# Kernel tuning notes

Measured on AMD Instinct MI355X. Metric: run time of the kernel, lower is better.

## Reference

```python
import jax, jax.numpy as jnp
import numpy as np

B, T, I, L, D, O = 256, 512, 512, 128, 4, 2
LN_EPS = 1e-5

def setup_inputs() -> dict:
    key = jax.random.key(0)
    ks = jax.random.split(key, 7)
    x = jax.random.normal(ks[0], (B, T, I), jnp.float32)
    # Xavier-ish scaling keeps the recurrence numerically tame
    W_in = jax.random.normal(ks[1], (L, D, I), jnp.float32) * (1.0 / np.sqrt(I))
    W_liquid = jax.random.normal(ks[2], (L, D, L), jnp.float32) * (1.0 / np.sqrt(L))
    W_gate = jax.random.normal(ks[3], (L, D), jnp.float32)
    b_liquid = jnp.zeros((L,), jnp.float32)
    W_out = jax.random.normal(ks[4], (O, L), jnp.float32) * (1.0 / np.sqrt(L))
    b_out = jnp.zeros((O,), jnp.float32)
    ln_w = jnp.ones((L,), jnp.float32)
    ln_b = jnp.zeros((L,), jnp.float32)
    leaky_rate = jnp.asarray(0.3, jnp.float32)
    return {"x": x, "W_in": W_in, "W_liquid": W_liquid, "W_gate": W_gate,
            "b_liquid": b_liquid, "W_out": W_out, "b_out": b_out,
            "ln_w": ln_w, "ln_b": ln_b, "leaky_rate": leaky_rate}

def reference(x, W_in, W_liquid, W_gate, b_liquid, W_out, b_out, ln_w, ln_b, leaky_rate):
    # Liquid dendritic RNN. Dropout is identity (eval mode).
    gate = jax.nn.sigmoid(W_gate)                                   # [L,D]
    # Input branch has no recurrent dependency -> batch it over all timesteps
    in_br = jax.nn.relu(jnp.einsum('ldi,bti->btld', W_in, x))       # [B,T,L,D]
    merged_in = jnp.einsum('btld,ld->btl', in_br, gate)             # [B,T,L]
    alpha = jax.nn.sigmoid(leaky_rate)

    def step(state, m_in_t):                                        # state [B,L]
        rec_br = jax.nn.relu(jnp.einsum('ldh,bh->bld', W_liquid, state))
        merged_rec = jnp.einsum('bld,ld->bl', rec_br, gate)
        li = m_in_t + merged_rec + b_liquid                         # [B,L]
        mu = jnp.mean(li, axis=-1, keepdims=True)
        var = jnp.var(li, axis=-1, keepdims=True)
        li = (li - mu) * jax.lax.rsqrt(var + LN_EPS) * ln_w + ln_b
        new_state = (1.0 - alpha) * state + alpha * jnp.tanh(li)
        return new_state, None

    state0 = jnp.zeros((x.shape[0], W_in.shape[0]), x.dtype)
    final_state, _ = jax.lax.scan(step, state0, jnp.swapaxes(merged_in, 0, 1))
    return final_state @ W_out.T + b_out                            # [B,O]
```

## Files before the change

kernel.cpp:

```cpp
#include <hip/hip_runtime.h>
#include <hip/hip_bf16.h>
#include <stdint.h>


typedef __bf16 bf16x8 __attribute__((ext_vector_type(8)));
typedef float f32x4_t __attribute__((ext_vector_type(4)));

__device__ inline unsigned short f2bf(float f) {
    union { float f; unsigned u; } v; v.f = f;
    unsigned r = v.u + 0x7fffu + ((v.u >> 16) & 1u);
    return (unsigned short)(r >> 16);
}

__device__ inline void lds_barrier() {
    asm volatile("s_waitcnt lgkmcnt(0)" ::: "memory");
    __builtin_amdgcn_s_barrier();
}

__global__ __launch_bounds__(256, 2)
void gemm_in_kernel(const float* __restrict__ x, const float* __restrict__ W_in,
                    const float* __restrict__ W_gate, const float* __restrict__ b_liq,
                    float* __restrict__ mt)
{
    __shared__ unsigned short As[128 * 32];
    __shared__ unsigned short Bs[128 * 32];

    const int tid = threadIdx.x;
    const int m0 = blockIdx.y * 128;
    const int n0 = blockIdx.x * 128;
    const int lane = tid & 63;
    const int wid  = tid >> 6;
    const int wr = wid >> 1, wc = wid & 1;
    const int fr = lane & 15, fq = lane >> 4;

    f32x4_t acc[4][4];
    #pragma unroll
    for (int i = 0; i < 4; ++i)
        #pragma unroll
        for (int j = 0; j < 4; ++j)
            acc[i][j] = (f32x4_t){0.f, 0.f, 0.f, 0.f};

    for (int k0 = 0; k0 < 512; k0 += 32) {
        #pragma unroll
        for (int p = 0; p < 4; ++p) {
            int ch = tid + p * 256;
            int r  = ch >> 3;
            int c  = ch & 7;
            float4 va = *(const float4*)(x    + (size_t)(m0 + r) * 512 + k0 + c * 4);
            float4 vb = *(const float4*)(W_in + (size_t)(n0 + r) * 512 + k0 + c * 4);
            ushort4 ha, hb;
            ha.x = f2bf(va.x); ha.y = f2bf(va.y); ha.z = f2bf(va.z); ha.w = f2bf(va.w);
            hb.x = f2bf(vb.x); hb.y = f2bf(vb.y); hb.z = f2bf(vb.z); hb.w = f2bf(vb.w);
            *(ushort4*)(&As[r * 32 + c * 4]) = ha;
            *(ushort4*)(&Bs[r * 32 + c * 4]) = hb;
        }
        __syncthreads();

        bf16x8 af[4], bfr[4];
        #pragma unroll
        for (int mi = 0; mi < 4; ++mi)
            af[mi] = *(const bf16x8*)(&As[(wr * 64 + mi * 16 + fr) * 32 + fq * 8]);
        #pragma unroll
        for (int ni = 0; ni < 4; ++ni)
            bfr[ni] = *(const bf16x8*)(&Bs[(wc * 64 + ni * 16 + fr) * 32 + fq * 8]);

        #pragma unroll
        for (int mi = 0; mi < 4; ++mi)
            #pragma unroll
            for (int ni = 0; ni < 4; ++ni)
                acc[mi][ni] = __builtin_amdgcn_mfma_f32_16x16x32_bf16(
                                  af[mi], bfr[ni], acc[mi][ni], 0, 0, 0);
        __syncthreads();
    }

    float gv[4], blq[4];
    #pragma unroll
    for (int ni = 0; ni < 4; ++ni) {
        int n = n0 + wc * 64 + ni * 16 + fr;
        gv[ni]  = 1.f / (1.f + __expf(-W_gate[n]));
        blq[ni] = b_liq[n >> 2];
    }
    #pragma unroll
    for (int mi = 0; mi < 4; ++mi) {
        #pragma unroll
        for (int ni = 0; ni < 4; ++ni) {
            int n = n0 + wc * 64 + ni * 16 + fr;
            int l = n >> 2;
            #pragma unroll
            for (int j = 0; j < 4; ++j) {
                float v = acc[mi][ni][j];
                float r = fmaxf(v, 0.f) * gv[ni];
                r += __shfl_xor(r, 1);
                r += __shfl_xor(r, 2);
                if ((lane & 3) == 0) {
                    int row = m0 + wr * 64 + mi * 16 + fq * 4 + j;
                    int bb = row >> 9;
                    int tt = row & 511;
                    mt[(size_t)bb * 65536 + (size_t)l * 512 + tt] = r + blq[ni];
                }
            }
        }
    }
}

__global__ __launch_bounds__(256, 1)
void scan_kernel(const float* __restrict__ mt, const float* __restrict__ W_liq,
                 const float* __restrict__ W_gate, const float* __restrict__ W_out,
                 const float* __restrict__ b_out, const float* __restrict__ ln_w,
                 const float* __restrict__ ln_b, const float* __restrict__ leaky,
                 float* __restrict__ out)
{
    __shared__ __align__(16) unsigned short s_bf[128];
    __shared__ __align__(16) float red2[8];
    __shared__ float s_final[128];

    const int tid  = threadIdx.x;
    const int b    = blockIdx.x;
    const int lane = tid & 63;
    const int w    = tid >> 6;
    const int fr   = lane & 15;
    const int fq   = lane >> 4;

    bf16x8 wfrag[8][4];
    #pragma unroll
    for (int mi = 0; mi < 8; ++mi) {
        const int n = w * 128 + mi * 16 + fr;
        const float gn = 1.f / (1.f + __expf(-W_gate[n]));
        const float* wrow = W_liq + (size_t)n * 128;
        #pragma unroll
        for (int kk = 0; kk < 4; ++kk) {
            float4 f0 = *(const float4*)(wrow + kk * 32 + fq * 8);
            float4 f1 = *(const float4*)(wrow + kk * 32 + fq * 8 + 4);
            union { unsigned short u[8]; bf16x8 v; } cv;
            cv.u[0] = f2bf(gn * f0.x); cv.u[1] = f2bf(gn * f0.y);
            cv.u[2] = f2bf(gn * f0.z); cv.u[3] = f2bf(gn * f0.w);
            cv.u[4] = f2bf(gn * f1.x); cv.u[5] = f2bf(gn * f1.y);
            cv.u[6] = f2bf(gn * f1.z); cv.u[7] = f2bf(gn * f1.w);
            wfrag[mi][kk] = cv.v;
        }
    }

    size_t midx[8];
    #pragma unroll
    for (int mi = 0; mi < 8; ++mi)
        midx[mi] = (size_t)b * 65536 + (size_t)(w * 32 + mi * 4 + fq) * 512;

    const int l_own  = w * 32 + (fr & 7) * 4 + fq;
    const float lw_o = ln_w[l_own];
    const float lb_o = ln_b[l_own];
    const float alpha = 1.f / (1.f + __expf(-leaky[0]));
    const float oma   = 1.f - alpha;

    float s_own = 0.f;

    float4 cur4[8], nxt4[8];
    #pragma unroll
    for (int mi = 0; mi < 8; ++mi) cur4[mi] = *(const float4*)(mt + midx[mi]);
    #pragma unroll
    for (int mi = 0; mi < 8; ++mi) nxt4[mi] = *(const float4*)(mt + midx[mi] + 4);

    if (tid < 64) ((unsigned*)s_bf)[tid] = 0u;
    lds_barrier();

    const f32x4_t z = {0.f, 0.f, 0.f, 0.f};

    for (int ts = 0; ts < 512; ts += 4) {
        float4 ld4[8];
        if (ts < 504) {
            #pragma unroll
            for (int mi = 0; mi < 8; ++mi)
                ld4[mi] = *(const float4*)(mt + midx[mi] + ts + 8);
        }

        #pragma unroll
        for (int ph = 0; ph < 4; ++ph) {
            bf16x8 bfr[4];
            #pragma unroll
            for (int kk = 0; kk < 4; ++kk)
                bfr[kk] = *(const bf16x8*)(&s_bf[kk * 32 + fq * 8]);

            f32x4_t a0[8], a1[8];
            #pragma unroll
            for (int mi = 0; mi < 8; ++mi) {
                a0[mi] = __builtin_amdgcn_mfma_f32_16x16x32_bf16(wfrag[mi][0], bfr[0], z, 0, 0, 0);
                a1[mi] = __builtin_amdgcn_mfma_f32_16x16x32_bf16(wfrag[mi][2], bfr[2], z, 0, 0, 0);
            }
            #pragma unroll
            for (int mi = 0; mi < 8; ++mi) {
                a0[mi] = __builtin_amdgcn_mfma_f32_16x16x32_bf16(wfrag[mi][1], bfr[1], a0[mi], 0, 0, 0);
                a1[mi] = __builtin_amdgcn_mfma_f32_16x16x32_bf16(wfrag[mi][3], bfr[3], a1[mi], 0, 0, 0);
            }

            float li[8], v1 = 0.f, v2 = 0.f;
            #pragma unroll
            for (int mi = 0; mi < 8; ++mi) {
                f32x4_t s4 = a0[mi] + a1[mi];
                float mr = (fmaxf(s4[0], 0.f) + fmaxf(s4[1], 0.f))
                         + (fmaxf(s4[2], 0.f) + fmaxf(s4[3], 0.f));
                li[mi] = cur4[mi][ph] + mr;
                v1 += li[mi];
                v2 = fmaf(li[mi], li[mi], v2);
            }
            v1 += __shfl_xor(v1, 16);  v2 += __shfl_xor(v2, 16);
            v1 += __shfl_xor(v1, 32);  v2 += __shfl_xor(v2, 32);
            if (lane == 0) { red2[2 * w] = v1; red2[2 * w + 1] = v2; }
            lds_barrier();

            float4 r0 = *(const float4*)&red2[0], r1 = *(const float4*)&red2[4];
            float S1 = (r0.x + r0.z) + (r1.x + r1.z);
            float S2 = (r0.y + r0.w) + (r1.y + r1.w);
            float mean = S1 * (1.f / 128.f);
            float var  = fmaf(-mean, mean, S2 * (1.f / 128.f));
            float rstd = __builtin_amdgcn_rsqf(var + 1e-5f);

            float sa = (fr & 1) ? li[1] : li[0];
            float sb = (fr & 1) ? li[3] : li[2];
            float sc = (fr & 1) ? li[5] : li[4];
            float sd = (fr & 1) ? li[7] : li[6];
            float se = (fr & 2) ? sb : sa;
            float sf = (fr & 2) ? sd : sc;
            float li_o = (fr & 4) ? sf : se;

            float t1 = rstd * lw_o;
            float xn = fmaf(li_o, t1, fmaf(-mean, t1, lb_o));
            float e  = __builtin_amdgcn_exp2f(xn * 2.8853900817779268f);
            float th = fmaf(-2.f, __builtin_amdgcn_rcpf(e + 1.f), 1.f);
            s_own = fmaf(oma, s_own, alpha * th);

            unsigned cvt;
            asm("v_cvt_pk_bf16_f32 %0, %1, %2" : "=v"(cvt) : "v"(s_own), "v"(0.f));
            if (fr < 8) s_bf[l_own] = (unsigned short)cvt;
            lds_barrier();
        }

        #pragma unroll
        for (int mi = 0; mi < 8; ++mi) cur4[mi] = nxt4[mi];
        if (ts < 504) {
            #pragma unroll
            for (int mi = 0; mi < 8; ++mi) nxt4[mi] = ld4[mi];
        }
    }

    if (fr < 8) s_final[l_own] = s_own;
    __syncthreads();
    if (tid < 2) {
        float accO = b_out[tid];
        #pragma unroll
        for (int h = 0; h < 128; ++h)
            accO = fmaf(s_final[h], W_out[tid * 128 + h], accO);
        out[b * 2 + tid] = accO;
    }
}

extern "C" void kernel_launch(void* const* d_in, const int* in_sizes, int n_in,
                              void* d_out, int out_size, void* d_ws, size_t ws_size,
                              hipStream_t stream)
{
    const float* x      = (const float*)d_in[0];
    const float* W_in   = (const float*)d_in[1];
    const float* W_liq  = (const float*)d_in[2];
    const float* W_gate = (const float*)d_in[3];
    const float* b_liq  = (const float*)d_in[4];
    const float* W_out  = (const float*)d_in[5];
    const float* b_out  = (const float*)d_in[6];
    const float* ln_w   = (const float*)d_in[7];
    const float* ln_b   = (const float*)d_in[8];
    const float* leaky  = (const float*)d_in[9];
    float* out = (float*)d_out;
    float* mt  = (float*)d_ws;

    gemm_in_kernel<<<dim3(4, 1024), 256, 0, stream>>>(x, W_in, W_gate, b_liq, mt);
    scan_kernel<<<256, 256, 0, stream>>>(mt, W_liq, W_gate,
                                         W_out, b_out, ln_w, ln_b, leaky, out);
}
```

Baseline: 676.5 us.

## Pack two batch rows per scan block with 512 threads

The scan kernel now processes two independent batch sequences per block, 8 waves split into two groups of 4, with per-group LDS state and reduction buffers. Grid size halves to 128 blocks of 512 threads, and launch bounds change to (512,2). The intent is to amortize the weight-fragment setup and improve latency hiding by interleaving two recurrences. In exchange, the barriers now synchronize both groups together, and the tighter register budget risks spilling the large resident weight fragments.

```diff
diff --git a/kernel.cpp b/kernel.cpp
--- a/kernel.cpp
+++ b/kernel.cpp
@@ -103,28 +103,30 @@
     }
 }
 
-__global__ __launch_bounds__(256, 1)
+__global__ __launch_bounds__(512, 2)
 void scan_kernel(const float* __restrict__ mt, const float* __restrict__ W_liq,
                  const float* __restrict__ W_gate, const float* __restrict__ W_out,
                  const float* __restrict__ b_out, const float* __restrict__ ln_w,
                  const float* __restrict__ ln_b, const float* __restrict__ leaky,
                  float* __restrict__ out)
 {
-    __shared__ __align__(16) unsigned short s_bf[128];
-    __shared__ __align__(16) float red2[8];
-    __shared__ float s_final[128];
+    __shared__ __align__(16) unsigned short s_bf[2][128];
+    __shared__ __align__(16) float red2[2][8];
+    __shared__ float s_final[2][128];
 
     const int tid  = threadIdx.x;
-    const int b    = blockIdx.x;
     const int lane = tid & 63;
     const int w    = tid >> 6;
+    const int wv   = w & 3;
+    const int grp  = w >> 2;
+    const int bb   = blockIdx.x * 2 + grp;
     const int fr   = lane & 15;
     const int fq   = lane >> 4;
 
     bf16x8 wfrag[8][4];
     #pragma unroll
     for (int mi = 0; mi < 8; ++mi) {
-        const int n = w * 128 + mi * 16 + fr;
+        const int n = wv * 128 + mi * 16 + fr;
         const float gn = 1.f / (1.f + __expf(-W_gate[n]));
         const float* wrow = W_liq + (size_t)n * 128;
         #pragma unroll
@@ -143,9 +145,9 @@
     size_t midx[8];
     #pragma unroll
     for (int mi = 0; mi < 8; ++mi)
-        midx[mi] = (size_t)b * 65536 + (size_t)(w * 32 + mi * 4 + fq) * 512;
-
-    const int l_own  = w * 32 + (fr & 7) * 4 + fq;
+        midx[mi] = (size_t)bb * 65536 + (size_t)(wv * 32 + mi * 4 + fq) * 512;
+
+    const int l_own  = wv * 32 + (fr & 7) * 4 + fq;
     const float lw_o = ln_w[l_own];
     const float lb_o = ln_b[l_own];
     const float alpha = 1.f / (1.f + __expf(-leaky[0]));
@@ -159,7 +161,7 @@
     #pragma unroll
     for (int mi = 0; mi < 8; ++mi) nxt4[mi] = *(const float4*)(mt + midx[mi] + 4);
 
-    if (tid < 64) ((unsigned*)s_bf)[tid] = 0u;
+    if (tid < 128) ((unsigned*)s_bf)[tid] = 0u;
     lds_barrier();
 
     const f32x4_t z = {0.f, 0.f, 0.f, 0.f};
@@ -177,7 +179,7 @@
             bf16x8 bfr[4];
             #pragma unroll
             for (int kk = 0; kk < 4; ++kk)
-                bfr[kk] = *(const bf16x8*)(&s_bf[kk * 32 + fq * 8]);
+                bfr[kk] = *(const bf16x8*)(&s_bf[grp][kk * 32 + fq * 8]);
 
             f32x4_t a0[8], a1[8];
             #pragma unroll
@@ -203,10 +205,10 @@
             }
             v1 += __shfl_xor(v1, 16);  v2 += __shfl_xor(v2, 16);
             v1 += __shfl_xor(v1, 32);  v2 += __shfl_xor(v2, 32);
-            if (lane == 0) { red2[2 * w] = v1; red2[2 * w + 1] = v2; }
+            if (lane == 0) { red2[grp][2 * wv] = v1; red2[grp][2 * wv + 1] = v2; }
             lds_barrier();
 
-            float4 r0 = *(const float4*)&red2[0], r1 = *(const float4*)&red2[4];
+            float4 r0 = *(const float4*)&red2[grp][0], r1 = *(const float4*)&red2[grp][4];
             float S1 = (r0.x + r0.z) + (r1.x + r1.z);
             float S2 = (r0.y + r0.w) + (r1.y + r1.w);
             float mean = S1 * (1.f / 128.f);
@@ -229,7 +231,7 @@
 
             unsigned cvt;
             asm("v_cvt_pk_bf16_f32 %0, %1, %2" : "=v"(cvt) : "v"(s_own), "v"(0.f));
-            if (fr < 8) s_bf[l_own] = (unsigned short)cvt;
+            if (fr < 8) s_bf[grp][l_own] = (unsigned short)cvt;
             lds_barrier();
         }
 
@@ -241,14 +243,14 @@
         }
     }
 
-    if (fr < 8) s_final[l_own] = s_own;
+    if (fr < 8) s_final[grp][l_own] = s_own;
     __syncthreads();
-    if (tid < 2) {
-        float accO = b_out[tid];
+    if (wv == 0 && lane < 2) {
+        float accO = b_out[lane];
         #pragma unroll
         for (int h = 0; h < 128; ++h)
-            accO = fmaf(s_final[h], W_out[tid * 128 + h], accO);
-        out[b * 2 + tid] = accO;
+            accO = fmaf(s_final[grp][h], W_out[lane * 128 + h], accO);
+        out[bb * 2 + lane] = accO;
     }
 }
 
@@ -270,6 +272,6 @@
     float* mt  = (float*)d_ws;
 
     gemm_in_kernel<<<dim3(4, 1024), 256, 0, stream>>>(x, W_in, W_gate, b_liq, mt);
-    scan_kernel<<<256, 256, 0, stream>>>(mt, W_liq, W_gate,
+    scan_kernel<<<128, 512, 0, stream>>>(mt, W_liq, W_gate,
                                          W_out, b_out, ln_w, ln_b, leaky, out);
 }
```

After: 1.531 ms. 2.26x slower.
